# Kernel optimization log

Measured on AMD Instinct MI355X. Metric: run time of the kernel, lower is better.

## Reference

```python
import jax, jax.numpy as jnp
import numpy as np

B, T, N = 16, 1024, 128
WIN, STEP = 30, 2
MOMENT_ORDERS = (2, 4, 8)
D_MODEL = 256


def _mask_diag(corr):
    n = corr.shape[-1]
    eye = jnp.eye(n, dtype=corr.dtype)
    return corr * (1.0 - eye) + eye


def corrcoef_time(xw):
    # xw: [..., L, N] -> corr over channels: [..., N, N]
    L = xw.shape[-2]
    xm = xw - xw.mean(axis=-2, keepdims=True)
    cov = jnp.einsum('...ln,...lm->...nm', xm, xm) / (L - 1 + 1e-8)
    var = jnp.clip(jnp.diagonal(cov, axis1=-2, axis2=-1), 1e-8, None)
    std = jnp.sqrt(var)
    corr = cov / (std[..., :, None] * std[..., None, :])
    corr = jnp.nan_to_num(corr, nan=0.0, posinf=0.0, neginf=0.0)
    return _mask_diag(corr)


def rowwise_corr(M):
    # M: [B, N, F]
    Xc = M - M.mean(axis=-1, keepdims=True)
    num = jnp.einsum('bnf,bmf->bnm', Xc, Xc)
    den1 = jnp.sqrt(jnp.clip((Xc ** 2).sum(axis=-1), 1e-8, None))
    corr = num / (den1[:, :, None] * den1[:, None, :])
    corr = jnp.nan_to_num(corr, nan=0.0, posinf=0.0, neginf=0.0)
    return _mask_diag(corr)


def layer_norm(x, gamma, beta, eps=1e-5):
    mu = x.mean(axis=-1, keepdims=True)
    var = ((x - mu) ** 2).mean(axis=-1, keepdims=True)
    return (x - mu) / jnp.sqrt(var + eps) * gamma + beta


def normalize_adj(adj):
    n = adj.shape[-1]
    A_hat = adj + jnp.eye(n, dtype=adj.dtype)
    d = A_hat.sum(axis=-1)
    dis = jnp.sqrt(1.0 / jnp.clip(d, 1e-8, None))
    return A_hat * dis[:, :, None] * dis[:, None, :]


def setup_inputs() -> dict:
    key = jax.random.key(0)
    ks = jax.random.split(key, 8)
    in_dim = len(MOMENT_ORDERS) * N
    return {
        'x': jax.random.normal(ks[0], (B, T, N), dtype=jnp.float32),
        'ln_gamma': jnp.ones((in_dim,), jnp.float32),
        'ln_beta': jnp.zeros((in_dim,), jnp.float32),
        'W1': jax.random.normal(ks[1], (in_dim, D_MODEL), jnp.float32) * 0.05,
        'b1': jnp.zeros((D_MODEL,), jnp.float32),
        'W2': jax.random.normal(ks[2], (D_MODEL, D_MODEL), jnp.float32) * 0.05,
        'b2': jnp.zeros((D_MODEL,), jnp.float32),
        'Wc': jax.random.normal(ks[3], (D_MODEL, 1), jnp.float32) * 0.05,
        'bc': jnp.zeros((1,), jnp.float32),
    }


def reference(x, ln_gamma, ln_beta, W1, b1, W2, b2, Wc, bc):
    # sliding windows (static indices)
    starts = np.arange(0, T - WIN + 1, STEP)
    idx = starts[:, None] + np.arange(WIN)[None, :]
    xw = x[:, idx, :]
    lo = corrcoef_time(xw)                            # [B, Wn, N, N]

    mean_lo = lo.mean(axis=1, keepdims=True)
    centered = lo - mean_lo
    cm_list, ho_list = [], []
    for d in MOMENT_ORDERS:
        cm = jnp.nan_to_num((centered ** d).mean(axis=1),
                            nan=0.0, posinf=0.0, neginf=0.0)  # [B, N, N]
        cm_list.append(cm)
        ho_list.append(rowwise_corr(cm))

    X = jnp.concatenate(cm_list, axis=-1)             # [B, N, 3N]
    X = layer_norm(X, ln_gamma, ln_beta)

    A = jnp.stack(ho_list, axis=1).mean(axis=1)
    A = 0.5 * (A + jnp.swapaxes(A, 1, 2))
    A_norm = normalize_adj(A)

    H = jax.nn.relu(jnp.einsum('bnm,bmd->bnd', A_norm, X @ W1 + b1))
    H = jax.nn.relu(jnp.einsum('bnm,bmd->bnd', A_norm, H @ W2 + b2))
    g = H.mean(axis=1)                                # [B, d_model]
    out = jax.nn.sigmoid(g @ Wc + bc)                 # [B, 1]
    return out
```

## Files before the change

### kernel.cpp

```cpp
#include <hip/hip_runtime.h>
#include <math.h>

#define BB  16
#define TT  1024
#define NN  128
#define WIN 30
#define NWD 498
#define DM  256
#define IND 384
#define GW  9

#define INV_W (1.0f/498.0f)

#define SARR (BB*NN*NN)

#define OFF_A     0
#define OFF_G     (OFF_A    + BB*NWD*NN)
#define OFF_CM2   (OFF_G    + BB*NWD*NN)
#define OFF_CM4   (OFF_CM2  + SARR)
#define OFF_CM8   (OFF_CM4  + SARR)
#define OFF_AD    (OFF_CM8  + SARR)
#define OFF_PART  (OFF_AD   + 3*SARR)
#define OFF_ANORM OFF_PART
#define OFF_BUFA  (OFF_ANORM + SARR)
#define OFF_BUFB  (OFF_BUFA + BB*NN*DM)

__global__ __launch_bounds__(128) void k1_stats(const float* __restrict__ x, float* __restrict__ ws) {
    int bx = blockIdx.x;
    int c = bx & 15, b = bx >> 4;
    int w0 = c*32, w1 = min(NWD, w0+32);
    int n = threadIdx.x;
    const float* xp = x + (size_t)b*TT*NN + n;

    float sum = 0.f, sq = 0.f;
    for (int t = 2*w0; t < 2*w0 + WIN; ++t) {
        float v = xp[(size_t)t*NN];
        sum += v; sq = fmaf(v, v, sq);
    }
    for (int w = w0; w < w1; ++w) {
        if (w > w0) {
            float o0 = xp[(size_t)(2*w-2)*NN], o1 = xp[(size_t)(2*w-1)*NN];
            float n0 = xp[(size_t)(2*w+28)*NN], n1 = xp[(size_t)(2*w+29)*NN];
            sum += (n0 + n1) - (o0 + o1);
            sq  += (n0*n0 + n1*n1) - (o0*o0 + o1*o1);
        }
        float mean = sum * (1.0f/30.0f);
        float ss = sq - 30.0f*mean*mean;
        float var = fmaxf(ss * (1.0f/29.0f), 1e-8f);
        float a = (1.0f / sqrtf(var)) * 0.185695338f;
        ws[OFF_A + ((size_t)b*NWD + w)*NN + n] = a;
        ws[OFF_G + ((size_t)b*NWD + w)*NN + n] = mean * a * 5.477225575f;
    }
}

__global__ __launch_bounds__(256) __attribute__((amdgpu_waves_per_eu(3, 3)))
void k24_inc(const float* __restrict__ x, float* __restrict__ ws) {
    __shared__ __align__(16) float xr[64][NN];
    __shared__ __align__(16) float sa[GW][NN];
    __shared__ __align__(16) float sg[GW][NN];
    int bx = blockIdx.x;
    int wc = bx & 7;
    int slab = (bx >> 3) % 6;
    int b = bx / 48;
    const char IS[6] = {0,0,0,0,1,1};
    const char JS[6] = {0,1,2,3,2,3};
    int is = IS[slab], js = JS[slab];
    int w0 = wc * 63, w1 = min(NWD, w0 + 63);
    int tid = threadIdx.x;
    int jg = tid & 7, ig = tid >> 3;
    int i0 = is*64 + ig*2;
    int j0 = js*32 + jg*4;

    const float* xb = x + (size_t)b*TT*NN;
    const float* Ab = ws + OFF_A + (size_t)b*NWD*NN;
    const float* Gb = ws + OFF_G + (size_t)b*NWD*NN;

    float P[2][4];
    float S1[2][4], S2[2][4], S3[2][4], S4[2][4], S5[2][4], S6[2][4], S7[2][4], S8[2][4];
#pragma unroll
    for (int p=0;p<2;++p)
#pragma unroll
        for (int q=0;q<4;++q) {
            P[p][q]=0.f;
            S1[p][q]=0.f;S2[p][q]=0.f;S3[p][q]=0.f;S4[p][q]=0.f;
            S5[p][q]=0.f;S6[p][q]=0.f;S7[p][q]=0.f;S8[p][q]=0.f;
        }

    auto moments = [&](int k) {
        float2 ai = *(const float2*)&sa[k][i0];
        float2 gi = *(const float2*)&sg[k][i0];
        float4 aj = *(const float4*)&sa[k][j0];
        float4 gj = *(const float4*)&sg[k][j0];
        float av[2] = {ai.x, ai.y};
        float mg[2] = {-gi.x, -gi.y};
        float aw[4] = {aj.x, aj.y, aj.z, aj.w};
        float gw[4] = {gj.x, gj.y, gj.z, gj.w};
#pragma unroll
        for (int p=0;p<2;++p)
#pragma unroll
            for (int q=0;q<4;++q) {
                float aa  = av[p]*aw[q];
                float ngg = mg[p]*gw[q];
                float c   = fmaf(P[p][q], aa, ngg);
                float c2 = c*c;
                float c3 = c2*c;
                float c4 = c2*c2;
                S1[p][q] += c;
                S2[p][q] += c2;
                S3[p][q] += c3;
                S4[p][q] += c4;
                S5[p][q] = fmaf(c4, c,  S5[p][q]);
                S6[p][q] = fmaf(c3, c3, S6[p][q]);
                S7[p][q] = fmaf(c3, c4, S7[p][q]);
                S8[p][q] = fmaf(c4, c4, S8[p][q]);
            }
    };

    int rlo = 2*w0;
    for (int wg = w0; wg < w1; wg += GW) {
        int m = min(GW, w1 - wg);
        __syncthreads();
        int rhi = 2*(wg + m - 1) + 29;
        int nr = rhi - rlo + 1;
        for (int idx = tid; idx < nr*32; idx += 256) {
            int r = idx >> 5, c4 = idx & 31;
            int t = rlo + r;
            *(float4*)&xr[t & 63][c4*4] = ((const float4*)(xb + (size_t)t*NN))[c4];
        }
        for (int idx = tid; idx < m*32; idx += 256) {
            int k = idx >> 5, c4 = idx & 31;
            *(float4*)&sa[k][c4*4] = ((const float4*)(Ab + (size_t)(wg+k)*NN))[c4];
        }
        for (int idx = tid; idx < m*32; idx += 256) {
            int k = idx >> 5, c4 = idx & 31;
            *(float4*)&sg[k][c4*4] = ((const float4*)(Gb + (size_t)(wg+k)*NN))[c4];
        }
        rlo = rhi + 1;
        __syncthreads();

        int kstart = 0;
        if (wg == w0) {
#pragma unroll 6
            for (int k = 0; k < WIN; ++k) {
                int t = 2*w0 + k;
                float2 xi = *(const float2*)&xr[t & 63][i0];
                float4 xj = *(const float4*)&xr[t & 63][j0];
                float av[2] = {xi.x, xi.y};
                float bv[4] = {xj.x, xj.y, xj.z, xj.w};
#pragma unroll
                for (int p=0;p<2;++p)
#pragma unroll
                    for (int q=0;q<4;++q) P[p][q] = fmaf(av[p], bv[q], P[p][q]);
            }
            moments(0);
            kstart = 1;
        }
        for (int k = kstart; k < m; ++k) {
            int w = wg + k;
            int tr[4] = {2*w - 2, 2*w - 1, 2*w + 28, 2*w + 29};
#pragma unroll
            for (int kk = 0; kk < 4; ++kk) {
                int t = tr[kk];
                float sgn = (kk < 2) ? -1.0f : 1.0f;
                float2 xi = *(const float2*)&xr[t & 63][i0];
                float4 xj = *(const float4*)&xr[t & 63][j0];
                float av[2] = {sgn*xi.x, sgn*xi.y};
                float bv[4] = {xj.x, xj.y, xj.z, xj.w};
#pragma unroll
                for (int p=0;p<2;++p)
#pragma unroll
                    for (int q=0;q<4;++q) P[p][q] = fmaf(av[p], bv[q], P[p][q]);
            }
            moments(k);
        }
    }

    float* tp = ws + OFF_PART + (size_t)bx*16384 + tid*8;
#define STORE_ARR(A, S) \
    *(float4*)&tp[(A)*2048]     = make_float4(S[0][0], S[0][1], S[0][2], S[0][3]); \
    *(float4*)&tp[(A)*2048 + 4] = make_float4(S[1][0], S[1][1], S[1][2], S[1][3]);
    STORE_ARR(0, S1) STORE_ARR(1, S2) STORE_ARR(2, S3) STORE_ARR(3, S4)
    STORE_ARR(4, S5) STORE_ARR(5, S6) STORE_ARR(6, S7) STORE_ARR(7, S8)
#undef STORE_ARR
}

__global__ __launch_bounds__(256) void kred(float* __restrict__ ws) {
    int pair = blockIdx.x >> 3, sub = blockIdx.x & 7;
    int b = pair / 6, slab = pair % 6;
    const char IS[6] = {0,0,0,0,1,1};
    const char JS[6] = {0,1,2,3,2,3};
    int is = IS[slab], js = JS[slab];
    int off = sub*256 + threadIdx.x;
    const float* base = ws + OFF_PART + (size_t)(b*48 + slab*8)*16384;

    float E[8];
#pragma unroll
    for (int a=0;a<8;++a) E[a] = 0.f;
    for (int c = 0; c < 8; ++c) {
        const float* tp = base + (size_t)c*16384;
#pragma unroll
        for (int a=0;a<8;++a) E[a] += tp[a*2048 + off];
    }

    int tid_old = off >> 3, e = off & 7;
    int ig = tid_old >> 3, jg = tid_old & 7;
    int p = e >> 2, q = e & 3;
    int i = is*64 + ig*2 + p;
    int j = js*32 + jg*4 + q;

    float cm2, cm4, cm8;
    if (i == j) {
        cm2 = 0.f; cm4 = 0.f; cm8 = 0.f;
    } else {
        float e1 = E[0]*INV_W, e2 = E[1]*INV_W, e3 = E[2]*INV_W, e4 = E[3]*INV_W;
        float e5 = E[4]*INV_W, e6 = E[5]*INV_W, e7 = E[6]*INV_W, e8 = E[7]*INV_W;
        float m  = e1;
        float m2 = m*m, m3 = m2*m, m4 = m2*m2, m5 = m4*m, m6 = m3*m3, m8 = m4*m4;
        cm2 = e2 - m2;
        cm4 = e4 - 4.f*m*e3 + 6.f*m2*e2 - 3.f*m4;
        cm8 = e8 - 8.f*m*e7 + 28.f*m2*e6 - 56.f*m3*e5 + 70.f*m4*e4
                 - 56.f*m5*e3 + 28.f*m6*e2 - 7.f*m8;
    }
    float* C2 = ws + OFF_CM2 + (size_t)b*NN*NN;
    float* C4 = ws + OFF_CM4 + (size_t)b*NN*NN;
    float* C8 = ws + OFF_CM8 + (size_t)b*NN*NN;
    C2[i*NN + j] = cm2; C2[j*NN + i] = cm2;
    C4[i*NN + j] = cm4; C4[j*NN + i] = cm4;
    C8[i*NN + j] = cm8; C8[j*NN + i] = cm8;
}

__global__ __launch_bounds__(256) void k5_rowcorr(float* __restrict__ ws) {
    __shared__ float Xc[NN][NN+1];
    __shared__ float rmn[NN];
    __shared__ float iden[NN];
    int t = blockIdx.x;
    int jh = t & 1; int di = (t >> 1) % 3; int b = t / 6;
    const float* cm = ws + (di==0 ? OFF_CM2 : (di==1 ? OFF_CM4 : OFF_CM8)) + (size_t)b*NN*NN;
    int tid = threadIdx.x;
    for (int idx = tid; idx < NN*NN; idx += 256) {
        int n = idx >> 7, f = idx & 127;
        Xc[n][f] = cm[idx];
    }
    __syncthreads();
    if (tid < NN) {
        float s = 0.f;
        for (int f = 0; f < NN; ++f) s += Xc[tid][f];
        rmn[tid] = s * (1.0f/NN);
    }
    __syncthreads();
    for (int idx = tid; idx < NN*NN; idx += 256) {
        int n = idx >> 7, f = idx & 127;
        Xc[n][f] -= rmn[n];
    }
    __syncthreads();
    if (tid < NN) {
        float s = 0.f;
        for (int f = 0; f < NN; ++f) { float v = Xc[tid][f]; s = fmaf(v, v, s); }
        iden[tid] = 1.0f/sqrtf(fmaxf(s, 1e-8f));
    }
    __syncthreads();
    int n0 = (tid >> 4)*8, m0 = jh*64 + (tid & 15)*4;
    float acc[8][4];
#pragma unroll
    for (int k=0;k<8;++k)
#pragma unroll
        for (int l=0;l<4;++l) acc[k][l] = 0.f;
    for (int f = 0; f < NN; ++f) {
        float an[8], am[4];
#pragma unroll
        for (int k=0;k<8;++k) an[k] = Xc[n0+k][f];
#pragma unroll
        for (int l=0;l<4;++l) am[l] = Xc[m0+l][f];
#pragma unroll
        for (int k=0;k<8;++k)
#pragma unroll
            for (int l=0;l<4;++l) acc[k][l] = fmaf(an[k], am[l], acc[k][l]);
    }
    float* Ad = ws + OFF_AD + (size_t)(b*3 + di)*NN*NN;
#pragma unroll
    for (int k=0;k<8;++k)
#pragma unroll
        for (int l=0;l<4;++l) {
            int gi = n0+k, gj = m0+l;
            float v = acc[k][l]*iden[gi]*iden[gj];
            if (gi == gj) v = 1.0f;
            Ad[gi*NN + gj] = v;
        }
}

__global__ __launch_bounds__(256) void k6_anorm(float* __restrict__ ws) {
    __shared__ float As[NN][NN+1];
    __shared__ float dis[NN];
    int b = blockIdx.x;
    const float* A0 = ws + OFF_AD + (size_t)(b*3 + 0)*NN*NN;
    const float* A1 = ws + OFF_AD + (size_t)(b*3 + 1)*NN*NN;
    const float* A2 = ws + OFF_AD + (size_t)(b*3 + 2)*NN*NN;
    int tid = threadIdx.x;
    for (int idx = tid; idx < NN*NN; idx += 256) {
        int n = idx >> 7, m = idx & 127;
        int ji = m*NN + n;
        float s = A0[idx] + A0[ji] + A1[idx] + A1[ji] + A2[idx] + A2[ji];
        As[n][m] = s * (1.0f/6.0f);
    }
    __syncthreads();
    if (tid < NN) {
        float d = 1.0f;
        for (int m = 0; m < NN; ++m) d += As[tid][m];
        dis[tid] = sqrtf(1.0f / fmaxf(d, 1e-8f));
    }
    __syncthreads();
    float* An = ws + OFF_ANORM + (size_t)b*NN*NN;
    for (int idx = tid; idx < NN*NN; idx += 256) {
        int n = idx >> 7, m = idx & 127;
        float v = As[n][m] + (n==m ? 1.0f : 0.0f);
        An[idx] = v * dis[n] * dis[m];
    }
}

__global__ __launch_bounds__(256) void k78_lngemm(const float* __restrict__ gamma, const float* __restrict__ beta,
                                                  const float* __restrict__ W1, const float* __restrict__ b1,
                                                  float* __restrict__ ws) {
    __shared__ float Xs[8][IND];
    __shared__ float smean[8], srstd[8];
    int r0 = blockIdx.x * 8;
    int tid = threadIdx.x;
    for (int r = 0; r < 8; ++r) {
        int row = r0 + r;
        int b = row >> 7, n = row & 127;
        const float* c2 = ws + OFF_CM2 + ((size_t)b*NN + n)*NN;
        const float* c4 = ws + OFF_CM4 + ((size_t)b*NN + n)*NN;
        const float* c8 = ws + OFF_CM8 + ((size_t)b*NN + n)*NN;
        for (int c = tid; c < IND; c += 256)
            Xs[r][c] = (c < 128) ? c2[c] : (c < 256) ? c4[c-128] : c8[c-256];
    }
    __syncthreads();
    {
        int team = tid >> 5, lane = tid & 31;
        float s = 0.f;
        for (int c = lane; c < IND; c += 32) s += Xs[team][c];
#pragma unroll
        for (int o = 16; o > 0; o >>= 1) s += __shfl_down(s, o, 32);
        float mean = __shfl(s, 0, 32) * (1.0f/IND);
        float v = 0.f;
        for (int c = lane; c < IND; c += 32) { float d = Xs[team][c] - mean; v = fmaf(d, d, v); }
#pragma unroll
        for (int o = 16; o > 0; o >>= 1) v += __shfl_down(v, o, 32);
        if (lane == 0) {
            smean[team] = mean;
            srstd[team] = 1.0f / sqrtf(v*(1.0f/IND) + 1e-5f);
        }
    }
    __syncthreads();
    for (int r = 0; r < 8; ++r) {
        float mean = smean[r], rstd = srstd[r];
        for (int c = tid; c < IND; c += 256)
            Xs[r][c] = (Xs[r][c] - mean)*rstd*gamma[c] + beta[c];
    }
    __syncthreads();
    float acc[8];
    float bv = b1[tid];
#pragma unroll
    for (int r = 0; r < 8; ++r) acc[r] = bv;
#pragma unroll 4
    for (int k = 0; k < IND; ++k) {
        float wv = W1[(size_t)k*DM + tid];
#pragma unroll
        for (int r = 0; r < 8; ++r) acc[r] = fmaf(Xs[r][k], wv, acc[r]);
    }
    float* O = ws + OFF_BUFA;
#pragma unroll
    for (int r = 0; r < 8; ++r) O[(size_t)(r0+r)*DM + tid] = acc[r];
}

__global__ __launch_bounds__(256) void k98_propgemm(const float* __restrict__ W2, const float* __restrict__ b2,
                                                    float* __restrict__ ws) {
    __shared__ float Ar[8][NN];
    __shared__ float Hs[8][DM];
    int bx = blockIdx.x;
    int b = bx >> 4, n0 = (bx & 15)*8;
    int tid = threadIdx.x;
    const float* A = ws + OFF_ANORM + (size_t)b*NN*NN;
    if (tid < NN) {
#pragma unroll
        for (int r = 0; r < 8; ++r) Ar[r][tid] = A[(n0+r)*NN + tid];
    }
    __syncthreads();
    float acc[8] = {0,0,0,0,0,0,0,0};
    const float* Z = ws + OFF_BUFA + (size_t)b*NN*DM;
#pragma unroll 4
    for (int m = 0; m < NN; ++m) {
        float z = Z[(size_t)m*DM + tid];
#pragma unroll
        for (int r = 0; r < 8; ++r) acc[r] = fmaf(Ar[r][m], z, acc[r]);
    }
#pragma unroll
    for (int r = 0; r < 8; ++r) Hs[r][tid] = fmaxf(acc[r], 0.0f);
    __syncthreads();
    float acc2[8];
    float bv = b2[tid];
#pragma unroll
    for (int r = 0; r < 8; ++r) acc2[r] = bv;
#pragma unroll 4
    for (int k = 0; k < DM; ++k) {
        float wv = W2[(size_t)k*DM + tid];
#pragma unroll
        for (int r = 0; r < 8; ++r) acc2[r] = fmaf(Hs[r][k], wv, acc2[r]);
    }
    float* O = ws + OFF_BUFB + (size_t)b*NN*DM;
#pragma unroll
    for (int r = 0; r < 8; ++r) O[(size_t)(n0+r)*DM + tid] = acc2[r];
}

__global__ __launch_bounds__(256) void k9_prop(float* __restrict__ ws) {
    __shared__ float Ar[8][NN];
    int bx = blockIdx.x;
    int b = bx >> 4, n0 = (bx & 15)*8;
    int tid = threadIdx.x;
    const float* A = ws + OFF_ANORM + (size_t)b*NN*NN;
    if (tid < NN) {
#pragma unroll
        for (int r = 0; r < 8; ++r) Ar[r][tid] = A[(n0+r)*NN + tid];
    }
    __syncthreads();
    float acc[8] = {0,0,0,0,0,0,0,0};
    const float* Z = ws + OFF_BUFB + (size_t)b*NN*DM;
#pragma unroll 4
    for (int m = 0; m < NN; ++m) {
        float z = Z[(size_t)m*DM + tid];
#pragma unroll
        for (int r = 0; r < 8; ++r) acc[r] = fmaf(Ar[r][m], z, acc[r]);
    }
    float* O = ws + OFF_BUFA + (size_t)b*NN*DM;
#pragma unroll
    for (int r = 0; r < 8; ++r) O[(size_t)(n0+r)*DM + tid] = fmaxf(acc[r], 0.0f);
}

__global__ __launch_bounds__(256) void k12_head(const float* __restrict__ Wc, const float* __restrict__ bc,
                                                float* __restrict__ ws, float* __restrict__ outp) {
    __shared__ float red[256];
    int b = blockIdx.x, tid = threadIdx.x;
    const float* H = ws + OFF_BUFA + (size_t)b*NN*DM;
    float s = 0.f;
    for (int n = 0; n < NN; ++n) s += H[(size_t)n*DM + tid];
    red[tid] = s * (1.0f/NN) * Wc[tid];
    __syncthreads();
    for (int o = 128; o > 0; o >>= 1) { if (tid < o) red[tid] += red[tid+o]; __syncthreads(); }
    if (tid == 0) outp[b] = 1.0f/(1.0f + expf(-(red[0] + bc[0])));
}

extern "C" void kernel_launch(void* const* d_in, const int* in_sizes, int n_in,
                              void* d_out, int out_size, void* d_ws, size_t ws_size,
                              hipStream_t stream) {
    (void)in_sizes; (void)n_in; (void)out_size; (void)ws_size;
    const float* x     = (const float*)d_in[0];
    const float* gamma = (const float*)d_in[1];
    const float* beta  = (const float*)d_in[2];
    const float* W1    = (const float*)d_in[3];
    const float* b1    = (const float*)d_in[4];
    const float* W2    = (const float*)d_in[5];
    const float* b2    = (const float*)d_in[6];
    const float* Wc    = (const float*)d_in[7];
    const float* bc    = (const float*)d_in[8];
    float* ws  = (float*)d_ws;
    float* out = (float*)d_out;

    k1_stats   <<<BB*16,   128, 0, stream>>>(x, ws);
    k24_inc    <<<BB*6*8,  256, 0, stream>>>(x, ws);
    kred       <<<BB*6*8,  256, 0, stream>>>(ws);
    k5_rowcorr <<<BB*3*2,  256, 0, stream>>>(ws);
    k6_anorm   <<<BB,      256, 0, stream>>>(ws);
    k78_lngemm <<<BB*NN/8, 256, 0, stream>>>(gamma, beta, W1, b1, ws);
    k98_propgemm<<<BB*16,  256, 0, stream>>>(W2, b2, ws);
    k9_prop    <<<BB*16,   256, 0, stream>>>(ws);
    k12_head   <<<BB,      256, 0, stream>>>(Wc, bc, ws, out);
}
```

Before: 278.8 us.

## Fuse post-reduction stages into one persistent kernel with grid barriers

Replaces the seven kernels after the moment accumulation (reduction, row correlation, adjacency normalization, LN+GEMM, two propagations, head) with one 512-block persistent kernel separated by atomic grid barriers. The goal is to remove launch gaps and tail effects between the many small dependent stages. It also runs the rowcorr and LN-GEMM stages concurrently on disjoint block ranges and changes per-block tile sizes (4 rows per propagation block, 16 rows per GEMM block). It relies on all 512 blocks being co-resident and adds a memset launch to reset the barrier counters; the single-block phases leave most of the grid idle at barriers.

```diff
diff --git a/kernel.cpp b/kernel.cpp
--- a/kernel.cpp
+++ b/kernel.cpp
@@ -9,6 +9,7 @@
 #define DM  256
 #define IND 384
 #define GW  9
+#define NB  512
 
 #define INV_W (1.0f/498.0f)
 
@@ -24,6 +25,7 @@
 #define OFF_ANORM OFF_PART
 #define OFF_BUFA  (OFF_ANORM + SARR)
 #define OFF_BUFB  (OFF_BUFA + BB*NN*DM)
+#define OFF_SYNC  (OFF_PART + 768*16384)
 
 __global__ __launch_bounds__(128) void k1_stats(const float* __restrict__ x, float* __restrict__ ws) {
     int bx = blockIdx.x;
@@ -184,268 +186,279 @@
 #undef STORE_ARR
 }
 
-__global__ __launch_bounds__(256) void kred(float* __restrict__ ws) {
-    int pair = blockIdx.x >> 3, sub = blockIdx.x & 7;
-    int b = pair / 6, slab = pair % 6;
+__device__ __forceinline__ void grid_barrier(unsigned* ctr, unsigned* gen) {
+    __syncthreads();
+    if (threadIdx.x == 0) {
+        unsigned g = __hip_atomic_load(gen, __ATOMIC_ACQUIRE, __HIP_MEMORY_SCOPE_AGENT);
+        unsigned a = __hip_atomic_fetch_add(ctr, 1u, __ATOMIC_ACQ_REL, __HIP_MEMORY_SCOPE_AGENT);
+        if (a == (unsigned)NB - 1u) {
+            __hip_atomic_store(ctr, 0u, __ATOMIC_RELAXED, __HIP_MEMORY_SCOPE_AGENT);
+            __hip_atomic_fetch_add(gen, 1u, __ATOMIC_ACQ_REL, __HIP_MEMORY_SCOPE_AGENT);
+        } else {
+            while (__hip_atomic_load(gen, __ATOMIC_ACQUIRE, __HIP_MEMORY_SCOPE_AGENT) == g)
+                __builtin_amdgcn_s_sleep(8);
+        }
+    }
+    __syncthreads();
+}
+
+__global__ __launch_bounds__(256) void kmega(const float* __restrict__ gamma, const float* __restrict__ beta,
+                                             const float* __restrict__ W1, const float* __restrict__ b1,
+                                             const float* __restrict__ W2, const float* __restrict__ b2,
+                                             const float* __restrict__ Wc, const float* __restrict__ bc,
+                                             float* __restrict__ ws, float* __restrict__ outp) {
+    __shared__ __align__(16) float smem[NN*(NN+1) + 2*NN];
+    unsigned* ctr = (unsigned*)(ws + OFF_SYNC);
+    unsigned* gen = ctr + 1;
+    int blk = blockIdx.x, tid = threadIdx.x;
     const char IS[6] = {0,0,0,0,1,1};
     const char JS[6] = {0,1,2,3,2,3};
-    int is = IS[slab], js = JS[slab];
-    int off = sub*256 + threadIdx.x;
-    const float* base = ws + OFF_PART + (size_t)(b*48 + slab*8)*16384;
-
-    float E[8];
-#pragma unroll
-    for (int a=0;a<8;++a) E[a] = 0.f;
-    for (int c = 0; c < 8; ++c) {
-        const float* tp = base + (size_t)c*16384;
-#pragma unroll
-        for (int a=0;a<8;++a) E[a] += tp[a*2048 + off];
-    }
-
-    int tid_old = off >> 3, e = off & 7;
-    int ig = tid_old >> 3, jg = tid_old & 7;
-    int p = e >> 2, q = e & 3;
-    int i = is*64 + ig*2 + p;
-    int j = js*32 + jg*4 + q;
-
-    float cm2, cm4, cm8;
-    if (i == j) {
-        cm2 = 0.f; cm4 = 0.f; cm8 = 0.f;
+
+    for (int idx = blk*256 + tid; idx < 96*2048; idx += NB*256) {
+        int slab_id = idx >> 11, off = idx & 2047;
+        int b = slab_id / 6, slab = slab_id % 6;
+        int is = IS[slab], js = JS[slab];
+        const float* base = ws + OFF_PART + (size_t)(b*48 + slab*8)*16384;
+        float E[8];
+#pragma unroll
+        for (int a=0;a<8;++a) E[a] = 0.f;
+        for (int c = 0; c < 8; ++c) {
+            const float* tp = base + (size_t)c*16384;
+#pragma unroll
+            for (int a=0;a<8;++a) E[a] += tp[a*2048 + off];
+        }
+        int tid_old = off >> 3, e = off & 7;
+        int ig = tid_old >> 3, jg = tid_old & 7;
+        int p = e >> 2, q = e & 3;
+        int i = is*64 + ig*2 + p;
+        int j = js*32 + jg*4 + q;
+        float cm2, cm4, cm8;
+        if (i == j) { cm2 = 0.f; cm4 = 0.f; cm8 = 0.f; }
+        else {
+            float e1 = E[0]*INV_W, e2 = E[1]*INV_W, e3 = E[2]*INV_W, e4 = E[3]*INV_W;
+            float e5 = E[4]*INV_W, e6 = E[5]*INV_W, e7 = E[6]*INV_W, e8 = E[7]*INV_W;
+            float m  = e1;
+            float m2 = m*m, m3 = m2*m, m4 = m2*m2, m5 = m4*m, m6 = m3*m3, m8 = m4*m4;
+            cm2 = e2 - m2;
+            cm4 = e4 - 4.f*m*e3 + 6.f*m2*e2 - 3.f*m4;
+            cm8 = e8 - 8.f*m*e7 + 28.f*m2*e6 - 56.f*m3*e5 + 70.f*m4*e4
+                     - 56.f*m5*e3 + 28.f*m6*e2 - 7.f*m8;
+        }
+        float* C2 = ws + OFF_CM2 + (size_t)b*NN*NN;
+        float* C4 = ws + OFF_CM4 + (size_t)b*NN*NN;
+        float* C8 = ws + OFF_CM8 + (size_t)b*NN*NN;
+        C2[i*NN + j] = cm2; C2[j*NN + i] = cm2;
+        C4[i*NN + j] = cm4; C4[j*NN + i] = cm4;
+        C8[i*NN + j] = cm8; C8[j*NN + i] = cm8;
+    }
+    grid_barrier(ctr, gen);
+
+    if (blk < 384) {
+        int jq = blk & 3, di = (blk >> 2) % 3, b = blk / 12;
+        float* Xc = smem;
+        float* rmn = smem + NN*(NN+1);
+        float* iden = rmn + NN;
+        const float* cm = ws + (di==0 ? OFF_CM2 : (di==1 ? OFF_CM4 : OFF_CM8)) + (size_t)b*NN*NN;
+        for (int idx = tid; idx < NN*NN; idx += 256) {
+            int n = idx >> 7, f = idx & 127;
+            Xc[n*(NN+1)+f] = cm[idx];
+        }
+        __syncthreads();
+        if (tid < NN) {
+            float s = 0.f;
+            for (int f = 0; f < NN; ++f) s += Xc[tid*(NN+1)+f];
+            rmn[tid] = s * (1.0f/NN);
+        }
+        __syncthreads();
+        for (int idx = tid; idx < NN*NN; idx += 256) {
+            int n = idx >> 7, f = idx & 127;
+            Xc[n*(NN+1)+f] -= rmn[n];
+        }
+        __syncthreads();
+        if (tid < NN) {
+            float s = 0.f;
+            for (int f = 0; f < NN; ++f) { float v = Xc[tid*(NN+1)+f]; s = fmaf(v, v, s); }
+            iden[tid] = 1.0f/sqrtf(fmaxf(s, 1e-8f));
+        }
+        __syncthreads();
+        int n0 = (tid >> 4)*8, m0 = jq*32 + (tid & 15)*2;
+        float acc[8][2];
+#pragma unroll
+        for (int k=0;k<8;++k) { acc[k][0]=0.f; acc[k][1]=0.f; }
+        for (int f = 0; f < NN; ++f) {
+            float am0 = Xc[(m0  )*(NN+1)+f];
+            float am1 = Xc[(m0+1)*(NN+1)+f];
+#pragma unroll
+            for (int k=0;k<8;++k) {
+                float an = Xc[(n0+k)*(NN+1)+f];
+                acc[k][0] = fmaf(an, am0, acc[k][0]);
+                acc[k][1] = fmaf(an, am1, acc[k][1]);
+            }
+        }
+        float* Ad = ws + OFF_AD + (size_t)(b*3 + di)*NN*NN;
+#pragma unroll
+        for (int k=0;k<8;++k)
+#pragma unroll
+            for (int l=0;l<2;++l) {
+                int gi = n0+k, gj = m0+l;
+                float v = acc[k][l]*iden[gi]*iden[gj];
+                if (gi == gj) v = 1.0f;
+                Ad[gi*NN + gj] = v;
+            }
     } else {
-        float e1 = E[0]*INV_W, e2 = E[1]*INV_W, e3 = E[2]*INV_W, e4 = E[3]*INV_W;
-        float e5 = E[4]*INV_W, e6 = E[5]*INV_W, e7 = E[6]*INV_W, e8 = E[7]*INV_W;
-        float m  = e1;
-        float m2 = m*m, m3 = m2*m, m4 = m2*m2, m5 = m4*m, m6 = m3*m3, m8 = m4*m4;
-        cm2 = e2 - m2;
-        cm4 = e4 - 4.f*m*e3 + 6.f*m2*e2 - 3.f*m4;
-        cm8 = e8 - 8.f*m*e7 + 28.f*m2*e6 - 56.f*m3*e5 + 70.f*m4*e4
-                 - 56.f*m5*e3 + 28.f*m6*e2 - 7.f*m8;
-    }
-    float* C2 = ws + OFF_CM2 + (size_t)b*NN*NN;
-    float* C4 = ws + OFF_CM4 + (size_t)b*NN*NN;
-    float* C8 = ws + OFF_CM8 + (size_t)b*NN*NN;
-    C2[i*NN + j] = cm2; C2[j*NN + i] = cm2;
-    C4[i*NN + j] = cm4; C4[j*NN + i] = cm4;
-    C8[i*NN + j] = cm8; C8[j*NN + i] = cm8;
-}
-
-__global__ __launch_bounds__(256) void k5_rowcorr(float* __restrict__ ws) {
-    __shared__ float Xc[NN][NN+1];
-    __shared__ float rmn[NN];
-    __shared__ float iden[NN];
-    int t = blockIdx.x;
-    int jh = t & 1; int di = (t >> 1) % 3; int b = t / 6;
-    const float* cm = ws + (di==0 ? OFF_CM2 : (di==1 ? OFF_CM4 : OFF_CM8)) + (size_t)b*NN*NN;
-    int tid = threadIdx.x;
-    for (int idx = tid; idx < NN*NN; idx += 256) {
-        int n = idx >> 7, f = idx & 127;
-        Xc[n][f] = cm[idx];
-    }
-    __syncthreads();
-    if (tid < NN) {
+        int r0 = (blk - 384) * 16;
+        float* Xs = smem;
+        float* sm = smem + 16*IND;
+        float* sr = sm + 16;
+        for (int r = 0; r < 16; ++r) {
+            int row = r0 + r;
+            int b = row >> 7, n = row & 127;
+            const float* c2 = ws + OFF_CM2 + ((size_t)b*NN + n)*NN;
+            const float* c4 = ws + OFF_CM4 + ((size_t)b*NN + n)*NN;
+            const float* c8 = ws + OFF_CM8 + ((size_t)b*NN + n)*NN;
+            for (int c = tid; c < IND; c += 256)
+                Xs[r*IND+c] = (c < 128) ? c2[c] : (c < 256) ? c4[c-128] : c8[c-256];
+        }
+        __syncthreads();
+        {
+            int team = tid >> 4, lane = tid & 15;
+            float s = 0.f;
+            for (int c = lane; c < IND; c += 16) s += Xs[team*IND + c];
+#pragma unroll
+            for (int o = 8; o > 0; o >>= 1) s += __shfl_down(s, o, 16);
+            float mean = __shfl(s, 0, 16) * (1.0f/IND);
+            float v = 0.f;
+            for (int c = lane; c < IND; c += 16) { float d = Xs[team*IND + c] - mean; v = fmaf(d, d, v); }
+#pragma unroll
+            for (int o = 8; o > 0; o >>= 1) v += __shfl_down(v, o, 16);
+            if (lane == 0) {
+                sm[team] = mean;
+                sr[team] = 1.0f / sqrtf(v*(1.0f/IND) + 1e-5f);
+            }
+        }
+        __syncthreads();
+        for (int r = 0; r < 16; ++r) {
+            float mean = sm[r], rstd = sr[r];
+            for (int c = tid; c < IND; c += 256)
+                Xs[r*IND+c] = (Xs[r*IND+c] - mean)*rstd*gamma[c] + beta[c];
+        }
+        __syncthreads();
+        float acc[16];
+        float bv = b1[tid];
+#pragma unroll
+        for (int r = 0; r < 16; ++r) acc[r] = bv;
+#pragma unroll 4
+        for (int k = 0; k < IND; ++k) {
+            float wv = W1[(size_t)k*DM + tid];
+#pragma unroll
+            for (int r = 0; r < 16; ++r) acc[r] = fmaf(Xs[r*IND+k], wv, acc[r]);
+        }
+        float* O = ws + OFF_BUFA;
+#pragma unroll
+        for (int r = 0; r < 16; ++r) O[(size_t)(r0+r)*DM + tid] = acc[r];
+    }
+    grid_barrier(ctr, gen);
+
+    if (blk < BB) {
+        int b = blk;
+        float* As = smem;
+        float* dis = smem + NN*(NN+1);
+        const float* A0 = ws + OFF_AD + (size_t)(b*3 + 0)*NN*NN;
+        const float* A1 = ws + OFF_AD + (size_t)(b*3 + 1)*NN*NN;
+        const float* A2 = ws + OFF_AD + (size_t)(b*3 + 2)*NN*NN;
+        for (int idx = tid; idx < NN*NN; idx += 256) {
+            int n = idx >> 7, m = idx & 127;
+            int ji = m*NN + n;
+            float s = A0[idx] + A0[ji] + A1[idx] + A1[ji] + A2[idx] + A2[ji];
+            As[n*(NN+1)+m] = s * (1.0f/6.0f);
+        }
+        __syncthreads();
+        if (tid < NN) {
+            float d = 1.0f;
+            for (int m = 0; m < NN; ++m) d += As[tid*(NN+1)+m];
+            dis[tid] = sqrtf(1.0f / fmaxf(d, 1e-8f));
+        }
+        __syncthreads();
+        float* An = ws + OFF_ANORM + (size_t)b*NN*NN;
+        for (int idx = tid; idx < NN*NN; idx += 256) {
+            int n = idx >> 7, m = idx & 127;
+            float v = As[n*(NN+1)+m] + (n==m ? 1.0f : 0.0f);
+            An[idx] = v * dis[n] * dis[m];
+        }
+    }
+    grid_barrier(ctr, gen);
+
+    {
+        int b = blk >> 5, n0 = (blk & 31)*4;
+        float* Ar = smem;
+        float* Hs = smem + 4*NN;
+        const float* A = ws + OFF_ANORM + (size_t)b*NN*NN;
+        if (tid < NN) {
+#pragma unroll
+            for (int r = 0; r < 4; ++r) Ar[r*NN + tid] = A[(n0+r)*NN + tid];
+        }
+        __syncthreads();
+        float acc[4] = {0,0,0,0};
+        const float* Z = ws + OFF_BUFA + (size_t)b*NN*DM;
+#pragma unroll 4
+        for (int m = 0; m < NN; ++m) {
+            float z = Z[(size_t)m*DM + tid];
+#pragma unroll
+            for (int r = 0; r < 4; ++r) acc[r] = fmaf(Ar[r*NN + m], z, acc[r]);
+        }
+#pragma unroll
+        for (int r = 0; r < 4; ++r) Hs[r*DM + tid] = fmaxf(acc[r], 0.0f);
+        __syncthreads();
+        float acc2[4];
+        float bv = b2[tid];
+#pragma unroll
+        for (int r = 0; r < 4; ++r) acc2[r] = bv;
+#pragma unroll 4
+        for (int k = 0; k < DM; ++k) {
+            float wv = W2[(size_t)k*DM + tid];
+#pragma unroll
+            for (int r = 0; r < 4; ++r) acc2[r] = fmaf(Hs[r*DM + k], wv, acc2[r]);
+        }
+        float* O = ws + OFF_BUFB + (size_t)b*NN*DM;
+#pragma unroll
+        for (int r = 0; r < 4; ++r) O[(size_t)(n0+r)*DM + tid] = acc2[r];
+    }
+    grid_barrier(ctr, gen);
+
+    {
+        int b = blk >> 5, n0 = (blk & 31)*4;
+        float* Ar = smem;
+        const float* A = ws + OFF_ANORM + (size_t)b*NN*NN;
+        if (tid < NN) {
+#pragma unroll
+            for (int r = 0; r < 4; ++r) Ar[r*NN + tid] = A[(n0+r)*NN + tid];
+        }
+        __syncthreads();
+        float acc[4] = {0,0,0,0};
+        const float* Z = ws + OFF_BUFB + (size_t)b*NN*DM;
+#pragma unroll 4
+        for (int m = 0; m < NN; ++m) {
+            float z = Z[(size_t)m*DM + tid];
+#pragma unroll
+            for (int r = 0; r < 4; ++r) acc[r] = fmaf(Ar[r*NN + m], z, acc[r]);
+        }
+        float* O = ws + OFF_BUFA + (size_t)b*NN*DM;
+#pragma unroll
+        for (int r = 0; r < 4; ++r) O[(size_t)(n0+r)*DM + tid] = fmaxf(acc[r], 0.0f);
+    }
+    grid_barrier(ctr, gen);
+
+    if (blk < BB) {
+        int b = blk;
+        float* red = smem;
+        const float* H = ws + OFF_BUFA + (size_t)b*NN*DM;
         float s = 0.f;
-        for (int f = 0; f < NN; ++f) s += Xc[tid][f];
-        rmn[tid] = s * (1.0f/NN);
-    }
-    __syncthreads();
-    for (int idx = tid; idx < NN*NN; idx += 256) {
-        int n = idx >> 7, f = idx & 127;
-        Xc[n][f] -= rmn[n];
-    }
-    __syncthreads();
-    if (tid < NN) {
-        float s = 0.f;
-        for (int f = 0; f < NN; ++f) { float v = Xc[tid][f]; s = fmaf(v, v, s); }
-        iden[tid] = 1.0f/sqrtf(fmaxf(s, 1e-8f));
-    }
-    __syncthreads();
-    int n0 = (tid >> 4)*8, m0 = jh*64 + (tid & 15)*4;
-    float acc[8][4];
-#pragma unroll
-    for (int k=0;k<8;++k)
-#pragma unroll
-        for (int l=0;l<4;++l) acc[k][l] = 0.f;
-    for (int f = 0; f < NN; ++f) {
-        float an[8], am[4];
-#pragma unroll
-        for (int k=0;k<8;++k) an[k] = Xc[n0+k][f];
-#pragma unroll
-        for (int l=0;l<4;++l) am[l] = Xc[m0+l][f];
-#pragma unroll
-        for (int k=0;k<8;++k)
-#pragma unroll
-            for (int l=0;l<4;++l) acc[k][l] = fmaf(an[k], am[l], acc[k][l]);
-    }
-    float* Ad = ws + OFF_AD + (size_t)(b*3 + di)*NN*NN;
-#pragma unroll
-    for (int k=0;k<8;++k)
-#pragma unroll
-        for (int l=0;l<4;++l) {
-            int gi = n0+k, gj = m0+l;
-            float v = acc[k][l]*iden[gi]*iden[gj];
-            if (gi == gj) v = 1.0f;
-            Ad[gi*NN + gj] = v;
-        }
-}
-
-__global__ __launch_bounds__(256) void k6_anorm(float* __restrict__ ws) {
-    __shared__ float As[NN][NN+1];
-    __shared__ float dis[NN];
-    int b = blockIdx.x;
-    const float* A0 = ws + OFF_AD + (size_t)(b*3 + 0)*NN*NN;
-    const float* A1 = ws + OFF_AD + (size_t)(b*3 + 1)*NN*NN;
-    const float* A2 = ws + OFF_AD + (size_t)(b*3 + 2)*NN*NN;
-    int tid = threadIdx.x;
-    for (int idx = tid; idx < NN*NN; idx += 256) {
-        int n = idx >> 7, m = idx & 127;
-        int ji = m*NN + n;
-        float s = A0[idx] + A0[ji] + A1[idx] + A1[ji] + A2[idx] + A2[ji];
-        As[n][m] = s * (1.0f/6.0f);
-    }
-    __syncthreads();
-    if (tid < NN) {
-        float d = 1.0f;
-        for (int m = 0; m < NN; ++m) d += As[tid][m];
-        dis[tid] = sqrtf(1.0f / fmaxf(d, 1e-8f));
-    }
-    __syncthreads();
-    float* An = ws + OFF_ANORM + (size_t)b*NN*NN;
-    for (int idx = tid; idx < NN*NN; idx += 256) {
-        int n = idx >> 7, m = idx & 127;
-        float v = As[n][m] + (n==m ? 1.0f : 0.0f);
-        An[idx] = v * dis[n] * dis[m];
-    }
-}
-
-__global__ __launch_bounds__(256) void k78_lngemm(const float* __restrict__ gamma, const float* __restrict__ beta,
-                                                  const float* __restrict__ W1, const float* __restrict__ b1,
-                                                  float* __restrict__ ws) {
-    __shared__ float Xs[8][IND];
-    __shared__ float smean[8], srstd[8];
-    int r0 = blockIdx.x * 8;
-    int tid = threadIdx.x;
-    for (int r = 0; r < 8; ++r) {
-        int row = r0 + r;
-        int b = row >> 7, n = row & 127;
-        const float* c2 = ws + OFF_CM2 + ((size_t)b*NN + n)*NN;
-        const float* c4 = ws + OFF_CM4 + ((size_t)b*NN + n)*NN;
-        const float* c8 = ws + OFF_CM8 + ((size_t)b*NN + n)*NN;
-        for (int c = tid; c < IND; c += 256)
-            Xs[r][c] = (c < 128) ? c2[c] : (c < 256) ? c4[c-128] : c8[c-256];
-    }
-    __syncthreads();
-    {
-        int team = tid >> 5, lane = tid & 31;
-        float s = 0.f;
-        for (int c = lane; c < IND; c += 32) s += Xs[team][c];
-#pragma unroll
-        for (int o = 16; o > 0; o >>= 1) s += __shfl_down(s, o, 32);
-        float mean = __shfl(s, 0, 32) * (1.0f/IND);
-        float v = 0.f;
-        for (int c = lane; c < IND; c += 32) { float d = Xs[team][c] - mean; v = fmaf(d, d, v); }
-#pragma unroll
-        for (int o = 16; o > 0; o >>= 1) v += __shfl_down(v, o, 32);
-        if (lane == 0) {
-            smean[team] = mean;
-            srstd[team] = 1.0f / sqrtf(v*(1.0f/IND) + 1e-5f);
-        }
-    }
-    __syncthreads();
-    for (int r = 0; r < 8; ++r) {
-        float mean = smean[r], rstd = srstd[r];
-        for (int c = tid; c < IND; c += 256)
-            Xs[r][c] = (Xs[r][c] - mean)*rstd*gamma[c] + beta[c];
-    }
-    __syncthreads();
-    float acc[8];
-    float bv = b1[tid];
-#pragma unroll
-    for (int r = 0; r < 8; ++r) acc[r] = bv;
-#pragma unroll 4
-    for (int k = 0; k < IND; ++k) {
-        float wv = W1[(size_t)k*DM + tid];
-#pragma unroll
-        for (int r = 0; r < 8; ++r) acc[r] = fmaf(Xs[r][k], wv, acc[r]);
-    }
-    float* O = ws + OFF_BUFA;
-#pragma unroll
-    for (int r = 0; r < 8; ++r) O[(size_t)(r0+r)*DM + tid] = acc[r];
-}
-
-__global__ __launch_bounds__(256) void k98_propgemm(const float* __restrict__ W2, const float* __restrict__ b2,
-                                                    float* __restrict__ ws) {
-    __shared__ float Ar[8][NN];
-    __shared__ float Hs[8][DM];
-    int bx = blockIdx.x;
-    int b = bx >> 4, n0 = (bx & 15)*8;
-    int tid = threadIdx.x;
-    const float* A = ws + OFF_ANORM + (size_t)b*NN*NN;
-    if (tid < NN) {
-#pragma unroll
-        for (int r = 0; r < 8; ++r) Ar[r][tid] = A[(n0+r)*NN + tid];
-    }
-    __syncthreads();
-    float acc[8] = {0,0,0,0,0,0,0,0};
-    const float* Z = ws + OFF_BUFA + (size_t)b*NN*DM;
-#pragma unroll 4
-    for (int m = 0; m < NN; ++m) {
-        float z = Z[(size_t)m*DM + tid];
-#pragma unroll
-        for (int r = 0; r < 8; ++r) acc[r] = fmaf(Ar[r][m], z, acc[r]);
-    }
-#pragma unroll
-    for (int r = 0; r < 8; ++r) Hs[r][tid] = fmaxf(acc[r], 0.0f);
-    __syncthreads();
-    float acc2[8];
-    float bv = b2[tid];
-#pragma unroll
-    for (int r = 0; r < 8; ++r) acc2[r] = bv;
-#pragma unroll 4
-    for (int k = 0; k < DM; ++k) {
-        float wv = W2[(size_t)k*DM + tid];
-#pragma unroll
-        for (int r = 0; r < 8; ++r) acc2[r] = fmaf(Hs[r][k], wv, acc2[r]);
-    }
-    float* O = ws + OFF_BUFB + (size_t)b*NN*DM;
-#pragma unroll
-    for (int r = 0; r < 8; ++r) O[(size_t)(n0+r)*DM + tid] = acc2[r];
-}
-
-__global__ __launch_bounds__(256) void k9_prop(float* __restrict__ ws) {
-    __shared__ float Ar[8][NN];
-    int bx = blockIdx.x;
-    int b = bx >> 4, n0 = (bx & 15)*8;
-    int tid = threadIdx.x;
-    const float* A = ws + OFF_ANORM + (size_t)b*NN*NN;
-    if (tid < NN) {
-#pragma unroll
-        for (int r = 0; r < 8; ++r) Ar[r][tid] = A[(n0+r)*NN + tid];
-    }
-    __syncthreads();
-    float acc[8] = {0,0,0,0,0,0,0,0};
-    const float* Z = ws + OFF_BUFB + (size_t)b*NN*DM;
-#pragma unroll 4
-    for (int m = 0; m < NN; ++m) {
-        float z = Z[(size_t)m*DM + tid];
-#pragma unroll
-        for (int r = 0; r < 8; ++r) acc[r] = fmaf(Ar[r][m], z, acc[r]);
-    }
-    float* O = ws + OFF_BUFA + (size_t)b*NN*DM;
-#pragma unroll
-    for (int r = 0; r < 8; ++r) O[(size_t)(n0+r)*DM + tid] = fmaxf(acc[r], 0.0f);
-}
-
-__global__ __launch_bounds__(256) void k12_head(const float* __restrict__ Wc, const float* __restrict__ bc,
-                                                float* __restrict__ ws, float* __restrict__ outp) {
-    __shared__ float red[256];
-    int b = blockIdx.x, tid = threadIdx.x;
-    const float* H = ws + OFF_BUFA + (size_t)b*NN*DM;
-    float s = 0.f;
-    for (int n = 0; n < NN; ++n) s += H[(size_t)n*DM + tid];
-    red[tid] = s * (1.0f/NN) * Wc[tid];
-    __syncthreads();
-    for (int o = 128; o > 0; o >>= 1) { if (tid < o) red[tid] += red[tid+o]; __syncthreads(); }
-    if (tid == 0) outp[b] = 1.0f/(1.0f + expf(-(red[0] + bc[0])));
+        for (int n = 0; n < NN; ++n) s += H[(size_t)n*DM + tid];
+        red[tid] = s * (1.0f/NN) * Wc[tid];
+        __syncthreads();
+        for (int o = 128; o > 0; o >>= 1) { if (tid < o) red[tid] += red[tid+o]; __syncthreads(); }
+        if (tid == 0) outp[b] = 1.0f/(1.0f + expf(-(red[0] + bc[0])));
+    }
 }
 
 extern "C" void kernel_launch(void* const* d_in, const int* in_sizes, int n_in,
@@ -464,13 +477,9 @@
     float* ws  = (float*)d_ws;
     float* out = (float*)d_out;
 
-    k1_stats   <<<BB*16,   128, 0, stream>>>(x, ws);
-    k24_inc    <<<BB*6*8,  256, 0, stream>>>(x, ws);
-    kred       <<<BB*6*8,  256, 0, stream>>>(ws);
-    k5_rowcorr <<<BB*3*2,  256, 0, stream>>>(ws);
-    k6_anorm   <<<BB,      256, 0, stream>>>(ws);
-    k78_lngemm <<<BB*NN/8, 256, 0, stream>>>(gamma, beta, W1, b1, ws);
-    k98_propgemm<<<BB*16,  256, 0, stream>>>(W2, b2, ws);
-    k9_prop    <<<BB*16,   256, 0, stream>>>(ws);
-    k12_head   <<<BB,      256, 0, stream>>>(Wc, bc, ws, out);
+    hipMemsetAsync(ws + OFF_SYNC, 0, 2*sizeof(unsigned), stream);
+
+    k1_stats <<<BB*16,  128, 0, stream>>>(x, ws);
+    k24_inc  <<<BB*6*8, 256, 0, stream>>>(x, ws);
+    kmega    <<<NB,     256, 0, stream>>>(gamma, beta, W1, b1, W2, b2, Wc, bc, ws, out);
 }
```

Result: slower. 1.103 ms (+295.6%).

## Merge row-correlation and LayerNorm-GEMM into one launch with finer row-corr split

Applied to the files above, without the earlier changes.

Combines the independent row-wise correlation kernel and the LayerNorm plus W1 GEMM kernel into a single launch, using block index ranges to pick the role, so both run concurrently and one launch is saved. The row-correlation work is also split four ways per matrix instead of two, doubling its block count to 192 for better occupancy on the many-CU GPU. The cost is redundant centering and normalization work per block, since each of the four blocks reloads the full 128x128 matrix. The shared buffer is sized for the larger row-corr use, which may lower occupancy for the GEMM blocks.

```diff
diff --git a/kernel.cpp b/kernel.cpp
--- a/kernel.cpp
+++ b/kernel.cpp
@@ -229,63 +229,116 @@
     C8[i*NN + j] = cm8; C8[j*NN + i] = cm8;
 }
 
-__global__ __launch_bounds__(256) void k5_rowcorr(float* __restrict__ ws) {
-    __shared__ float Xc[NN][NN+1];
-    __shared__ float rmn[NN];
-    __shared__ float iden[NN];
-    int t = blockIdx.x;
-    int jh = t & 1; int di = (t >> 1) % 3; int b = t / 6;
-    const float* cm = ws + (di==0 ? OFF_CM2 : (di==1 ? OFF_CM4 : OFF_CM8)) + (size_t)b*NN*NN;
-    int tid = threadIdx.x;
-    for (int idx = tid; idx < NN*NN; idx += 256) {
-        int n = idx >> 7, f = idx & 127;
-        Xc[n][f] = cm[idx];
-    }
-    __syncthreads();
-    if (tid < NN) {
-        float s = 0.f;
-        for (int f = 0; f < NN; ++f) s += Xc[tid][f];
-        rmn[tid] = s * (1.0f/NN);
-    }
-    __syncthreads();
-    for (int idx = tid; idx < NN*NN; idx += 256) {
-        int n = idx >> 7, f = idx & 127;
-        Xc[n][f] -= rmn[n];
-    }
-    __syncthreads();
-    if (tid < NN) {
-        float s = 0.f;
-        for (int f = 0; f < NN; ++f) { float v = Xc[tid][f]; s = fmaf(v, v, s); }
-        iden[tid] = 1.0f/sqrtf(fmaxf(s, 1e-8f));
-    }
-    __syncthreads();
-    int n0 = (tid >> 4)*8, m0 = jh*64 + (tid & 15)*4;
-    float acc[8][4];
-#pragma unroll
-    for (int k=0;k<8;++k)
-#pragma unroll
-        for (int l=0;l<4;++l) acc[k][l] = 0.f;
-    for (int f = 0; f < NN; ++f) {
-        float an[8], am[4];
-#pragma unroll
-        for (int k=0;k<8;++k) an[k] = Xc[n0+k][f];
-#pragma unroll
-        for (int l=0;l<4;++l) am[l] = Xc[m0+l][f];
+__global__ __launch_bounds__(256) void kB(const float* __restrict__ gamma, const float* __restrict__ beta,
+                                          const float* __restrict__ W1, const float* __restrict__ b1,
+                                          float* __restrict__ ws) {
+    __shared__ __align__(16) float smem[NN*(NN+1) + 2*NN];
+    int blk = blockIdx.x, tid = threadIdx.x;
+    if (blk < 192) {
+        int rem = blk % 12;
+        int b = blk / 12, di = rem >> 2, jq = rem & 3;
+        float* Xc  = smem;
+        float* rmn = smem + NN*(NN+1);
+        float* iden = rmn + NN;
+        const float* cm = ws + (di==0 ? OFF_CM2 : (di==1 ? OFF_CM4 : OFF_CM8)) + (size_t)b*NN*NN;
+        for (int idx = tid; idx < NN*NN; idx += 256) {
+            int n = idx >> 7, f = idx & 127;
+            Xc[n*(NN+1)+f] = cm[idx];
+        }
+        __syncthreads();
+        if (tid < NN) {
+            float s = 0.f;
+            for (int f = 0; f < NN; ++f) s += Xc[tid*(NN+1)+f];
+            rmn[tid] = s * (1.0f/NN);
+        }
+        __syncthreads();
+        for (int idx = tid; idx < NN*NN; idx += 256) {
+            int n = idx >> 7, f = idx & 127;
+            Xc[n*(NN+1)+f] -= rmn[n];
+        }
+        __syncthreads();
+        if (tid < NN) {
+            float s = 0.f;
+            for (int f = 0; f < NN; ++f) { float v = Xc[tid*(NN+1)+f]; s = fmaf(v, v, s); }
+            iden[tid] = 1.0f/sqrtf(fmaxf(s, 1e-8f));
+        }
+        __syncthreads();
+        int n0 = (tid >> 4)*8, m0 = jq*32 + (tid & 15)*2;
+        float acc[8][2];
+#pragma unroll
+        for (int k=0;k<8;++k) { acc[k][0]=0.f; acc[k][1]=0.f; }
+        for (int f = 0; f < NN; ++f) {
+            float am0 = Xc[(m0  )*(NN+1)+f];
+            float am1 = Xc[(m0+1)*(NN+1)+f];
+#pragma unroll
+            for (int k=0;k<8;++k) {
+                float an = Xc[(n0+k)*(NN+1)+f];
+                acc[k][0] = fmaf(an, am0, acc[k][0]);
+                acc[k][1] = fmaf(an, am1, acc[k][1]);
+            }
+        }
+        float* Ad = ws + OFF_AD + (size_t)(b*3 + di)*NN*NN;
 #pragma unroll
         for (int k=0;k<8;++k)
 #pragma unroll
-            for (int l=0;l<4;++l) acc[k][l] = fmaf(an[k], am[l], acc[k][l]);
-    }
-    float* Ad = ws + OFF_AD + (size_t)(b*3 + di)*NN*NN;
-#pragma unroll
-    for (int k=0;k<8;++k)
-#pragma unroll
-        for (int l=0;l<4;++l) {
-            int gi = n0+k, gj = m0+l;
-            float v = acc[k][l]*iden[gi]*iden[gj];
-            if (gi == gj) v = 1.0f;
-            Ad[gi*NN + gj] = v;
-        }
+            for (int l=0;l<2;++l) {
+                int gi = n0+k, gj = m0+l;
+                float v = acc[k][l]*iden[gi]*iden[gj];
+                if (gi == gj) v = 1.0f;
+                Ad[gi*NN + gj] = v;
+            }
+    } else {
+        int r0 = (blk - 192) * 8;
+        float* Xs = smem;
+        float* sm = smem + 8*IND;
+        float* sr = sm + 8;
+        for (int r = 0; r < 8; ++r) {
+            int row = r0 + r;
+            int b = row >> 7, n = row & 127;
+            const float* c2 = ws + OFF_CM2 + ((size_t)b*NN + n)*NN;
+            const float* c4 = ws + OFF_CM4 + ((size_t)b*NN + n)*NN;
+            const float* c8 = ws + OFF_CM8 + ((size_t)b*NN + n)*NN;
+            for (int c = tid; c < IND; c += 256)
+                Xs[r*IND+c] = (c < 128) ? c2[c] : (c < 256) ? c4[c-128] : c8[c-256];
+        }
+        __syncthreads();
+        {
+            int team = tid >> 5, lane = tid & 31;
+            float s = 0.f;
+            for (int c = lane; c < IND; c += 32) s += Xs[team*IND + c];
+#pragma unroll
+            for (int o = 16; o > 0; o >>= 1) s += __shfl_down(s, o, 32);
+            float mean = __shfl(s, 0, 32) * (1.0f/IND);
+            float v = 0.f;
+            for (int c = lane; c < IND; c += 32) { float d = Xs[team*IND + c] - mean; v = fmaf(d, d, v); }
+#pragma unroll
+            for (int o = 16; o > 0; o >>= 1) v += __shfl_down(v, o, 32);
+            if (lane == 0) {
+                sm[team] = mean;
+                sr[team] = 1.0f / sqrtf(v*(1.0f/IND) + 1e-5f);
+            }
+        }
+        __syncthreads();
+        for (int r = 0; r < 8; ++r) {
+            float mean = sm[r], rstd = sr[r];
+            for (int c = tid; c < IND; c += 256)
+                Xs[r*IND+c] = (Xs[r*IND+c] - mean)*rstd*gamma[c] + beta[c];
+        }
+        __syncthreads();
+        float acc[8];
+        float bv = b1[tid];
+#pragma unroll
+        for (int r = 0; r < 8; ++r) acc[r] = bv;
+#pragma unroll 4
+        for (int k = 0; k < IND; ++k) {
+            float wv = W1[(size_t)k*DM + tid];
+#pragma unroll
+            for (int r = 0; r < 8; ++r) acc[r] = fmaf(Xs[r*IND+k], wv, acc[r]);
+        }
+        float* O = ws + OFF_BUFA;
+#pragma unroll
+        for (int r = 0; r < 8; ++r) O[(size_t)(r0+r)*DM + tid] = acc[r];
+    }
 }
 
 __global__ __launch_bounds__(256) void k6_anorm(float* __restrict__ ws) {
@@ -315,61 +368,6 @@
         float v = As[n][m] + (n==m ? 1.0f : 0.0f);
         An[idx] = v * dis[n] * dis[m];
     }
-}
-
-__global__ __launch_bounds__(256) void k78_lngemm(const float* __restrict__ gamma, const float* __restrict__ beta,
-                                                  const float* __restrict__ W1, const float* __restrict__ b1,
-                                                  float* __restrict__ ws) {
-    __shared__ float Xs[8][IND];
-    __shared__ float smean[8], srstd[8];
-    int r0 = blockIdx.x * 8;
-    int tid = threadIdx.x;
-    for (int r = 0; r < 8; ++r) {
-        int row = r0 + r;
-        int b = row >> 7, n = row & 127;
-        const float* c2 = ws + OFF_CM2 + ((size_t)b*NN + n)*NN;
-        const float* c4 = ws + OFF_CM4 + ((size_t)b*NN + n)*NN;
-        const float* c8 = ws + OFF_CM8 + ((size_t)b*NN + n)*NN;
-        for (int c = tid; c < IND; c += 256)
-            Xs[r][c] = (c < 128) ? c2[c] : (c < 256) ? c4[c-128] : c8[c-256];
-    }
-    __syncthreads();
-    {
-        int team = tid >> 5, lane = tid & 31;
-        float s = 0.f;
-        for (int c = lane; c < IND; c += 32) s += Xs[team][c];
-#pragma unroll
-        for (int o = 16; o > 0; o >>= 1) s += __shfl_down(s, o, 32);
-        float mean = __shfl(s, 0, 32) * (1.0f/IND);
-        float v = 0.f;
-        for (int c = lane; c < IND; c += 32) { float d = Xs[team][c] - mean; v = fmaf(d, d, v); }
-#pragma unroll
-        for (int o = 16; o > 0; o >>= 1) v += __shfl_down(v, o, 32);
-        if (lane == 0) {
-            smean[team] = mean;
-            srstd[team] = 1.0f / sqrtf(v*(1.0f/IND) + 1e-5f);
-        }
-    }
-    __syncthreads();
-    for (int r = 0; r < 8; ++r) {
-        float mean = smean[r], rstd = srstd[r];
-        for (int c = tid; c < IND; c += 256)
-            Xs[r][c] = (Xs[r][c] - mean)*rstd*gamma[c] + beta[c];
-    }
-    __syncthreads();
-    float acc[8];
-    float bv = b1[tid];
-#pragma unroll
-    for (int r = 0; r < 8; ++r) acc[r] = bv;
-#pragma unroll 4
-    for (int k = 0; k < IND; ++k) {
-        float wv = W1[(size_t)k*DM + tid];
-#pragma unroll
-        for (int r = 0; r < 8; ++r) acc[r] = fmaf(Xs[r][k], wv, acc[r]);
-    }
-    float* O = ws + OFF_BUFA;
-#pragma unroll
-    for (int r = 0; r < 8; ++r) O[(size_t)(r0+r)*DM + tid] = acc[r];
 }
 
 __global__ __launch_bounds__(256) void k98_propgemm(const float* __restrict__ W2, const float* __restrict__ b2,
@@ -467,9 +465,8 @@
     k1_stats   <<<BB*16,   128, 0, stream>>>(x, ws);
     k24_inc    <<<BB*6*8,  256, 0, stream>>>(x, ws);
     kred       <<<BB*6*8,  256, 0, stream>>>(ws);
-    k5_rowcorr <<<BB*3*2,  256, 0, stream>>>(ws);
+    kB         <<<448,     256, 0, stream>>>(gamma, beta, W1, b1, ws);
     k6_anorm   <<<BB,      256, 0, stream>>>(ws);
-    k78_lngemm <<<BB*NN/8, 256, 0, stream>>>(gamma, beta, W1, b1, ws);
     k98_propgemm<<<BB*16,  256, 0, stream>>>(W2, b2, ws);
     k9_prop    <<<BB*16,   256, 0, stream>>>(ws);
     k12_head   <<<BB,      256, 0, stream>>>(Wc, bc, ws, out);
```

New measurement: 264.1 us. 5.3% less time.
